# Performance work log

Hardware: AMD Instinct MI355X
Metric: run time of the kernel (lower is better)

The kernel has to match this reference:

```python
import jax, jax.numpy as jnp
import numpy as np

NUM_CLASSES = 1000
DIM = 256
N = 400000
MOMENTUM = 0.9


def setup_inputs() -> dict:
    key = jax.random.key(0)
    k1, k2, k3 = jax.random.split(key, 3)
    grads = jax.random.normal(k1, (N, DIM), dtype=jnp.float32)
    labels = jax.random.randint(k2, (N,), 0, NUM_CLASSES)
    # centroids buffer in its steady (initialized=True) state
    centroids = jax.random.normal(k3, (NUM_CLASSES, DIM), dtype=jnp.float32) * 0.1
    return {"grads": grads, "labels": labels, "centroids": centroids}


def reference(grads, labels, centroids):
    # --- update_centroids: per-class masked mean + EMA, as one segment-reduce ---
    sums = jax.ops.segment_sum(grads, labels, num_segments=NUM_CLASSES)            # [C, D]
    counts = jax.ops.segment_sum(jnp.ones((grads.shape[0],), grads.dtype), labels,
                                 num_segments=NUM_CLASSES)                          # [C]
    class_means = sums / jnp.maximum(counts, 1.0)[:, None]                          # [C, D]
    present = (counts > 0)[:, None]
    new_centroids = jnp.where(present,
                              MOMENTUM * centroids + (1.0 - MOMENTUM) * class_means,
                              centroids)                                            # classes with no samples keep old centroid

    # --- purify: rank-1 projection removing the first principal direction ---
    centered = new_centroids - new_centroids.mean(axis=0, keepdims=True)            # [C, D]
    _, _, Vh = jnp.linalg.svd(centered, full_matrices=False)
    v_y = Vh[0]                                                                     # [D]
    proj = (grads @ v_y)[:, None] * v_y[None, :]                                    # [N, D]
    return grads - proj
```

## Files before the change

### kernel.cpp

```cpp
#include <hip/hip_runtime.h>

#define N_ROWS 400000
#define DIM 256
#define NCLS 1000
#define NSQ 8

#define NB_S 256
#define NT_S 512
#define NBE  64
#define NTE  1024
#define NB_P 2048
#define NT_P 256
#define TOTW_P (NB_P * (NT_P / 64))

typedef float f4 __attribute__((ext_vector_type(4)));

#define OFF_BAR     0
#define OFF_BAR2    64
#define OFF_COUNTS  1024
#define OFF_COLSUM  5120
#define OFF_MAXBUF  6144
#define ZERO_BYTES  6208
#define OFF_BASE    6208
#define OFF_CURSOR  10304
#define OFF_V       14400
#define OFF_IDX     15424
#define OFF_NC      1615424
#define OFF_NCT     2639424
#define OFF_MA      3663424
#define OFF_MB      3925568

template <int NBLK>
__device__ __forceinline__ void grid_bar(unsigned* bar, int& phase) {
  __syncthreads();
  if (threadIdx.x == 0) {
    ++phase;
    __threadfence();
    __hip_atomic_fetch_add(bar, 1u, __ATOMIC_RELAXED, __HIP_MEMORY_SCOPE_AGENT);
    const unsigned target = (unsigned)NBLK * (unsigned)phase;
    while (__hip_atomic_load(bar, __ATOMIC_RELAXED, __HIP_MEMORY_SCOPE_AGENT) < target)
      __builtin_amdgcn_s_sleep(8);
    __threadfence();
  }
  __syncthreads();
}

__global__ __launch_bounds__(NT_S) void k_sort(const int* __restrict__ labels,
                                               char* __restrict__ ws) {
  unsigned* bar    = (unsigned*)(ws + OFF_BAR);
  unsigned* counts = (unsigned*)(ws + OFF_COUNTS);
  unsigned* base   = (unsigned*)(ws + OFF_BASE);
  unsigned* cursor = (unsigned*)(ws + OFF_CURSOR);
  unsigned* idx    = (unsigned*)(ws + OFF_IDX);

  __shared__ unsigned su[1024];
  const int t = threadIdx.x, b = blockIdx.x;
  int phase = 0;

  for (int i = t; i < NCLS; i += NT_S) su[i] = 0u;
  __syncthreads();
  for (int i = b*NT_S + t; i < N_ROWS; i += NB_S*NT_S)
    atomicAdd(&su[labels[i]], 1u);
  __syncthreads();
  for (int i = t; i < NCLS; i += NT_S) { unsigned v = su[i]; if (v) atomicAdd(&counts[i], v); }
  grid_bar<NB_S>(bar, phase);

  if (b == 0) {
    su[t] = counts[t]; su[t+512] = counts[t+512];
    int offset = 1;
    for (int d = 512; d > 0; d >>= 1) {
      __syncthreads();
      if (t < d) { int ai = offset*(2*t+1)-1, bi = offset*(2*t+2)-1; su[bi] += su[ai]; }
      offset <<= 1;
    }
    __syncthreads();
    if (t == 0) su[1023] = 0u;
    for (int d = 1; d < 1024; d <<= 1) {
      offset >>= 1;
      __syncthreads();
      if (t < d) { int ai = offset*(2*t+1)-1, bi = offset*(2*t+2)-1;
                   unsigned tm = su[ai]; su[ai] = su[bi]; su[bi] += tm; }
    }
    __syncthreads();
    base[t] = su[t]; cursor[t] = su[t];
    base[t+512] = su[t+512]; cursor[t+512] = su[t+512];
  }
  grid_bar<NB_S>(bar, phase);

  for (int i = b*NT_S + t; i < N_ROWS; i += NB_S*NT_S) {
    unsigned p = atomicAdd(&cursor[labels[i]], 1u);
    idx[p] = (unsigned)i;
  }
}

__global__ __launch_bounds__(512) void k_reduce(const float* __restrict__ grads,
                                                const unsigned* __restrict__ idx,
                                                const unsigned* __restrict__ base,
                                                const unsigned* __restrict__ counts,
                                                const float* __restrict__ centroids,
                                                float* __restrict__ NC,
                                                float* __restrict__ NCT,
                                                float* __restrict__ colsum) {
  const int cls = blockIdx.x;
  const unsigned s0 = base[cls], n = counts[cls];
  const int wave = threadIdx.x >> 6, lane = threadIdx.x & 63;
  const float4* g4 = (const float4*)grads;
  float4 acc = make_float4(0.f, 0.f, 0.f, 0.f);
  unsigned u = (unsigned)wave;
  for (; u + 24 < n; u += 32) {
    unsigned r0 = idx[s0+u],    r1 = idx[s0+u+8];
    unsigned r2 = idx[s0+u+16], r3 = idx[s0+u+24];
    float4 a = g4[(size_t)r0*64 + lane];
    float4 c = g4[(size_t)r1*64 + lane];
    float4 d = g4[(size_t)r2*64 + lane];
    float4 e = g4[(size_t)r3*64 + lane];
    acc.x += (a.x + c.x) + (d.x + e.x);
    acc.y += (a.y + c.y) + (d.y + e.y);
    acc.z += (a.z + c.z) + (d.z + e.z);
    acc.w += (a.w + c.w) + (d.w + e.w);
  }
  for (; u < n; u += 8) {
    unsigned r0 = idx[s0+u];
    float4 a = g4[(size_t)r0*64 + lane];
    acc.x += a.x; acc.y += a.y; acc.z += a.z; acc.w += a.w;
  }
  __shared__ float4 tmp[8][64];
  tmp[wave][lane] = acc;
  __syncthreads();
  const int d = threadIdx.x;
  if (d < DIM) {
    const float* tf = (const float*)tmp;
    float s = 0.f;
    #pragma unroll
    for (int w2 = 0; w2 < 8; ++w2) s += tf[w2*256 + d];
    float mean = s / fmaxf((float)n, 1.0f);
    float ce = centroids[cls*DIM + d];
    float ncv = (n > 0u) ? (0.9f*ce + 0.1f*mean) : ce;
    NC[cls*DIM + d]  = ncv;
    NCT[d*NCLS + cls] = ncv;
    atomicAdd(&colsum[d], ncv);
  }
}

__global__ __launch_bounds__(NTE) void k_eigen(char* __restrict__ ws) {
  unsigned* bar2   = (unsigned*)(ws + OFF_BAR2);
  float*    colsum = (float*)(ws + OFF_COLSUM);
  unsigned* maxbuf = (unsigned*)(ws + OFF_MAXBUF);
  float*    vfin   = (float*)(ws + OFF_V);
  float*    NC     = (float*)(ws + OFF_NC);
  float*    NCT    = (float*)(ws + OFF_NCT);
  float*    MA     = (float*)(ws + OFF_MA);
  float*    MB     = (float*)(ws + OFF_MB);

  __shared__ float scol[4][NCLS];
  __shared__ float sf[4][NTE];
  __shared__ float sx[DIM], sy[DIM];
  __shared__ int   sidx[256];
  __shared__ unsigned smax;

  const int t = threadIdx.x, b = blockIdx.x;
  const int i = t & 255, h = t >> 8;
  int phase = 0;

  {
    #pragma unroll
    for (int q = 0; q < 4; ++q)
      if (t < NCLS) scol[q][t] = NCT[(size_t)(b + 64*q)*NCLS + t];
    if (t == 0) smax = 0u;
    __syncthreads();
    float a0 = 0.f, a1 = 0.f, a2 = 0.f, a3 = 0.f;
    const int k0 = h * 250;
    #pragma unroll 5
    for (int k = k0; k < k0 + 250; ++k) {
      float nv = NC[k*DIM + i];
      a0 += nv * scol[0][k]; a1 += nv * scol[1][k];
      a2 += nv * scol[2][k]; a3 += nv * scol[3][k];
    }
    sf[0][t] = a0; sf[1][t] = a1; sf[2][t] = a2; sf[3][t] = a3;
    __syncthreads();
    if (h == 0) {
      float am = 0.f;
      #pragma unroll
      for (int q = 0; q < 4; ++q) {
        const int j = b + 64*q;
        float v = sf[q][i]+sf[q][i+256]+sf[q][i+512]+sf[q][i+768]
                - colsum[i]*colsum[j]*(1.0f/NCLS);
        MA[j*DIM + i] = v;
        am = fmaxf(am, fabsf(v));
      }
      #pragma unroll
      for (int m = 1; m < 64; m <<= 1) am = fmaxf(am, __shfl_xor(am, m, 64));
      if ((t & 63) == 0) atomicMax(&smax, __float_as_uint(am));
    }
    __syncthreads();
    if (t == 0) atomicMax(maxbuf, smax);
  }
  grid_bar<NBE>(bar2, phase);

  for (int st = 0; st < NSQ; ++st) {
    const float* A = (st & 1) ? MB : MA;
    float*       C = (st & 1) ? MA : MB;
    const float inv = 1.0f / __uint_as_float(maxbuf[st]);
    #pragma unroll
    for (int q = 0; q < 4; ++q)
      if (t < DIM) scol[q][t] = A[(b + 64*q)*DIM + t];
    if (t == 0) smax = 0u;
    __syncthreads();
    float a0 = 0.f, a1 = 0.f, a2 = 0.f, a3 = 0.f;
    const int k0 = h * 64;
    #pragma unroll 8
    for (int k = k0; k < k0 + 64; ++k) {
      float av = A[k*DIM + i];
      a0 += av * scol[0][k]; a1 += av * scol[1][k];
      a2 += av * scol[2][k]; a3 += av * scol[3][k];
    }
    sf[0][t] = a0; sf[1][t] = a1; sf[2][t] = a2; sf[3][t] = a3;
    __syncthreads();
    if (h == 0) {
      float am = 0.f;
      #pragma unroll
      for (int q = 0; q < 4; ++q) {
        const int j = b + 64*q;
        float v = (sf[q][i]+sf[q][i+256]+sf[q][i+512]+sf[q][i+768]) * inv * inv;
        C[j*DIM + i] = v;
        am = fmaxf(am, fabsf(v));
      }
      #pragma unroll
      for (int m = 1; m < 64; m <<= 1) am = fmaxf(am, __shfl_xor(am, m, 64));
      if ((t & 63) == 0) atomicMax(&smax, __float_as_uint(am));
    }
    __syncthreads();
    if (t == 0) atomicMax(&maxbuf[st+1], smax);
    grid_bar<NBE>(bar2, phase);
  }

  if (b == 0) {
    const int k0 = h * 64;
    float ns = 0.f;
    for (int k = k0; k < k0 + 64; ++k) { float x = MA[k*DIM + i]; ns += x*x; }
    sf[0][t] = ns;
    __syncthreads();
    if (h == 0) {
      scol[0][i] = sf[0][i]+sf[0][i+256]+sf[0][i+512]+sf[0][i+768];
      sidx[i] = i;
    }
    __syncthreads();
    for (int s = 128; s > 0; s >>= 1) {
      if (t < s && scol[0][t+s] > scol[0][t]) { scol[0][t] = scol[0][t+s]; sidx[t] = sidx[t+s]; }
      __syncthreads();
    }
    const int jm = sidx[0];
    const float nrm = sqrtf(fmaxf(scol[0][0], 1e-30f));
    __syncthreads();
    if (t < DIM) sx[t] = MA[(size_t)jm*DIM + t] / nrm;
    __syncthreads();
    for (int it = 0; it < 3; ++it) {
      float a2 = 0.f;
      #pragma unroll 8
      for (int k = k0; k < k0 + 64; ++k) a2 += MA[k*DIM + i] * sx[k];
      sf[0][t] = a2;
      __syncthreads();
      if (h == 0) {
        float yv = sf[0][i]+sf[0][i+256]+sf[0][i+512]+sf[0][i+768];
        sy[i] = yv;
        float q = yv*yv;
        #pragma unroll
        for (int m = 1; m < 64; m <<= 1) q += __shfl_xor(q, m, 64);
        if ((i & 63) == 0) scol[0][i >> 6] = q;
      }
      __syncthreads();
      const float innrm = rsqrtf(fmaxf(scol[0][0]+scol[0][1]+scol[0][2]+scol[0][3], 1e-30f));
      if (t < DIM) sx[t] = sy[t] * innrm;
      __syncthreads();
    }
    if (t < DIM) vfin[t] = sx[t];
  }
}

__global__ __launch_bounds__(NT_P) void k_project(const f4* __restrict__ g4,
                                                  const float* __restrict__ v,
                                                  f4* __restrict__ out) {
  const int lane = threadIdx.x & 63;
  const f4 v4 = ((const f4*)v)[lane];
  const int w = blockIdx.x * (NT_P/64) + (threadIdx.x >> 6);
  int r = w;
  for (; r + TOTW_P < N_ROWS; r += 2*TOTW_P) {
    f4 a = __builtin_nontemporal_load(&g4[(size_t)r*64 + lane]);
    f4 c = __builtin_nontemporal_load(&g4[(size_t)(r+TOTW_P)*64 + lane]);
    float da = a.x*v4.x + a.y*v4.y + a.z*v4.z + a.w*v4.w;
    float db = c.x*v4.x + c.y*v4.y + c.z*v4.z + c.w*v4.w;
    #pragma unroll
    for (int m = 1; m < 64; m <<= 1) { da += __shfl_xor(da, m, 64); db += __shfl_xor(db, m, 64); }
    f4 o0 = a - da * v4;
    f4 o1 = c - db * v4;
    __builtin_nontemporal_store(o0, &out[(size_t)r*64 + lane]);
    __builtin_nontemporal_store(o1, &out[(size_t)(r+TOTW_P)*64 + lane]);
  }
  for (; r < N_ROWS; r += TOTW_P) {
    f4 a = __builtin_nontemporal_load(&g4[(size_t)r*64 + lane]);
    float da = a.x*v4.x + a.y*v4.y + a.z*v4.z + a.w*v4.w;
    #pragma unroll
    for (int m = 1; m < 64; m <<= 1) da += __shfl_xor(da, m, 64);
    f4 o = a - da * v4;
    __builtin_nontemporal_store(o, &out[(size_t)r*64 + lane]);
  }
}

extern "C" void kernel_launch(void* const* d_in, const int* in_sizes, int n_in,
                              void* d_out, int out_size, void* d_ws, size_t ws_size,
                              hipStream_t stream) {
  const float* grads     = (const float*)d_in[0];
  const int*   labels    = (const int*)d_in[1];
  const float* centroids = (const float*)d_in[2];
  float* out = (float*)d_out;
  char* ws = (char*)d_ws;

  unsigned* idx    = (unsigned*)(ws + OFF_IDX);
  unsigned* counts = (unsigned*)(ws + OFF_COUNTS);
  unsigned* base   = (unsigned*)(ws + OFF_BASE);
  float*    colsum = (float*)(ws + OFF_COLSUM);
  float*    vfin   = (float*)(ws + OFF_V);
  float*    NC     = (float*)(ws + OFF_NC);
  float*    NCT    = (float*)(ws + OFF_NCT);

  (void)hipMemsetAsync(ws, 0, ZERO_BYTES, stream);

  k_sort<<<NB_S, NT_S, 0, stream>>>(labels, ws);
  k_reduce<<<NCLS, 512, 0, stream>>>(grads, idx, base, counts, centroids, NC, NCT, colsum);
  k_eigen<<<NBE, NTE, 0, stream>>>(ws);
  k_project<<<NB_P, NT_P, 0, stream>>>((const f4*)grads, vfin, (f4*)out);
}
```

Baseline: 440.1 us.

## Cut squaring steps, add power-iteration polish, vectorize eigen kernel, drop colsum atomics

The repeated-squaring eigen solver goes from eight squarings to six, and the closing power iteration goes from three to eight steps, so fewer grid-wide barriers are needed. The eigen kernel's Gram and squaring matmuls now use float4 rows spread over 16 waves. Column sums are computed inside the eigen kernel rather than through 256k global atomics in the reduce kernel. The gather loads in the reduce kernel are marked nontemporal. With fewer squarings the spectral gap is amplified less, so the result leans more on the polish iterations to converge.

```diff
diff --git a/kernel.cpp b/kernel.cpp
--- a/kernel.cpp
+++ b/kernel.cpp
@@ -3,7 +3,8 @@
 #define N_ROWS 400000
 #define DIM 256
 #define NCLS 1000
-#define NSQ 8
+#define NSQ 6
+#define NPOLISH 8
 
 #define NB_S 256
 #define NT_S 512
@@ -18,7 +19,6 @@
 #define OFF_BAR     0
 #define OFF_BAR2    64
 #define OFF_COUNTS  1024
-#define OFF_COLSUM  5120
 #define OFF_MAXBUF  6144
 #define ZERO_BYTES  6208
 #define OFF_BASE    6208
@@ -99,32 +99,27 @@
                                                 const unsigned* __restrict__ counts,
                                                 const float* __restrict__ centroids,
                                                 float* __restrict__ NC,
-                                                float* __restrict__ NCT,
-                                                float* __restrict__ colsum) {
+                                                float* __restrict__ NCT) {
   const int cls = blockIdx.x;
   const unsigned s0 = base[cls], n = counts[cls];
   const int wave = threadIdx.x >> 6, lane = threadIdx.x & 63;
-  const float4* g4 = (const float4*)grads;
-  float4 acc = make_float4(0.f, 0.f, 0.f, 0.f);
+  const f4* g4 = (const f4*)grads;
+  f4 acc = {0.f, 0.f, 0.f, 0.f};
   unsigned u = (unsigned)wave;
   for (; u + 24 < n; u += 32) {
     unsigned r0 = idx[s0+u],    r1 = idx[s0+u+8];
     unsigned r2 = idx[s0+u+16], r3 = idx[s0+u+24];
-    float4 a = g4[(size_t)r0*64 + lane];
-    float4 c = g4[(size_t)r1*64 + lane];
-    float4 d = g4[(size_t)r2*64 + lane];
-    float4 e = g4[(size_t)r3*64 + lane];
-    acc.x += (a.x + c.x) + (d.x + e.x);
-    acc.y += (a.y + c.y) + (d.y + e.y);
-    acc.z += (a.z + c.z) + (d.z + e.z);
-    acc.w += (a.w + c.w) + (d.w + e.w);
+    f4 a = __builtin_nontemporal_load(&g4[(size_t)r0*64 + lane]);
+    f4 c = __builtin_nontemporal_load(&g4[(size_t)r1*64 + lane]);
+    f4 d = __builtin_nontemporal_load(&g4[(size_t)r2*64 + lane]);
+    f4 e = __builtin_nontemporal_load(&g4[(size_t)r3*64 + lane]);
+    acc += (a + c) + (d + e);
   }
   for (; u < n; u += 8) {
     unsigned r0 = idx[s0+u];
-    float4 a = g4[(size_t)r0*64 + lane];
-    acc.x += a.x; acc.y += a.y; acc.z += a.z; acc.w += a.w;
-  }
-  __shared__ float4 tmp[8][64];
+    acc += __builtin_nontemporal_load(&g4[(size_t)r0*64 + lane]);
+  }
+  __shared__ f4 tmp[8][64];
   tmp[wave][lane] = acc;
   __syncthreads();
   const int d = threadIdx.x;
@@ -138,13 +133,11 @@
     float ncv = (n > 0u) ? (0.9f*ce + 0.1f*mean) : ce;
     NC[cls*DIM + d]  = ncv;
     NCT[d*NCLS + cls] = ncv;
-    atomicAdd(&colsum[d], ncv);
   }
 }
 
 __global__ __launch_bounds__(NTE) void k_eigen(char* __restrict__ ws) {
   unsigned* bar2   = (unsigned*)(ws + OFF_BAR2);
-  float*    colsum = (float*)(ws + OFF_COLSUM);
   unsigned* maxbuf = (unsigned*)(ws + OFF_MAXBUF);
   float*    vfin   = (float*)(ws + OFF_V);
   float*    NC     = (float*)(ws + OFF_NC);
@@ -152,128 +145,171 @@
   float*    MA     = (float*)(ws + OFF_MA);
   float*    MB     = (float*)(ws + OFF_MB);
 
-  __shared__ float scol[4][NCLS];
-  __shared__ float sf[4][NTE];
-  __shared__ float sx[DIM], sy[DIM];
+  __shared__ float scol[4][1024];
+  __shared__ f4    sacc[4][16][64];
+  __shared__ f4    scs[16][64];
+  __shared__ float colsumv[256];
+  __shared__ float red[256];
   __shared__ int   sidx[256];
+  __shared__ float sx[256], sy[256];
   __shared__ unsigned smax;
 
   const int t = threadIdx.x, b = blockIdx.x;
-  const int i = t & 255, h = t >> 8;
+  const int wave = t >> 6, lane = t & 63;
   int phase = 0;
-
+  const f4* NC4 = (const f4*)NC;
+
+  #pragma unroll
+  for (int q = 0; q < 4; ++q)
+    for (int k = t; k < NCLS; k += NTE) scol[q][k] = NCT[(size_t)(b + 64*q)*NCLS + k];
+  if (t == 0) smax = 0u;
+  __syncthreads();
   {
-    #pragma unroll
-    for (int q = 0; q < 4; ++q)
-      if (t < NCLS) scol[q][t] = NCT[(size_t)(b + 64*q)*NCLS + t];
-    if (t == 0) smax = 0u;
-    __syncthreads();
-    float a0 = 0.f, a1 = 0.f, a2 = 0.f, a3 = 0.f;
-    const int k0 = h * 250;
-    #pragma unroll 5
-    for (int k = k0; k < k0 + 250; ++k) {
-      float nv = NC[k*DIM + i];
+    f4 a0 = {0,0,0,0}, a1 = {0,0,0,0}, a2 = {0,0,0,0}, a3 = {0,0,0,0}, cs = {0,0,0,0};
+    for (int k = wave; k < NCLS; k += 16) {
+      f4 nv = NC4[(size_t)k*64 + lane];
       a0 += nv * scol[0][k]; a1 += nv * scol[1][k];
       a2 += nv * scol[2][k]; a3 += nv * scol[3][k];
-    }
-    sf[0][t] = a0; sf[1][t] = a1; sf[2][t] = a2; sf[3][t] = a3;
-    __syncthreads();
-    if (h == 0) {
-      float am = 0.f;
+      cs += nv;
+    }
+    sacc[0][wave][lane] = a0; sacc[1][wave][lane] = a1;
+    sacc[2][wave][lane] = a2; sacc[3][wave][lane] = a3;
+    scs[wave][lane] = cs;
+  }
+  __syncthreads();
+  float c0 = 0, c1 = 0, c2 = 0, c3 = 0;
+  if (t < 256) {
+    const float* p0 = (const float*)sacc[0]; const float* p1 = (const float*)sacc[1];
+    const float* p2 = (const float*)sacc[2]; const float* p3 = (const float*)sacc[3];
+    const float* pc = (const float*)scs;
+    float cc = 0;
+    #pragma unroll
+    for (int w2 = 0; w2 < 16; ++w2) {
+      c0 += p0[w2*256 + t]; c1 += p1[w2*256 + t];
+      c2 += p2[w2*256 + t]; c3 += p3[w2*256 + t];
+      cc += pc[w2*256 + t];
+    }
+    colsumv[t] = cc;
+  }
+  __syncthreads();
+  if (t < 256) {
+    const float inC = 1.0f / NCLS;
+    const float cst = colsumv[t];
+    float v0 = c0 - cst*colsumv[b      ]*inC;
+    float v1 = c1 - cst*colsumv[b +  64]*inC;
+    float v2 = c2 - cst*colsumv[b + 128]*inC;
+    float v3 = c3 - cst*colsumv[b + 192]*inC;
+    MA[(size_t)(b      )*DIM + t] = v0;
+    MA[(size_t)(b +  64)*DIM + t] = v1;
+    MA[(size_t)(b + 128)*DIM + t] = v2;
+    MA[(size_t)(b + 192)*DIM + t] = v3;
+    float am = fmaxf(fmaxf(fabsf(v0), fabsf(v1)), fmaxf(fabsf(v2), fabsf(v3)));
+    #pragma unroll
+    for (int m = 1; m < 64; m <<= 1) am = fmaxf(am, __shfl_xor(am, m, 64));
+    if ((t & 63) == 0) atomicMax(&smax, __float_as_uint(am));
+  }
+  __syncthreads();
+  if (t == 0) atomicMax(maxbuf, smax);
+  grid_bar<NBE>(bar2, phase);
+
+  for (int st = 0; st < NSQ; ++st) {
+    const float* A = (st & 1) ? MB : MA;
+    float*       C = (st & 1) ? MA : MB;
+    const f4* A4 = (const f4*)A;
+    const float inv = 1.0f / __uint_as_float(maxbuf[st]);
+    if (t < 256) {
+      scol[0][t] = A[(size_t)(b      )*DIM + t];
+      scol[1][t] = A[(size_t)(b +  64)*DIM + t];
+      scol[2][t] = A[(size_t)(b + 128)*DIM + t];
+      scol[3][t] = A[(size_t)(b + 192)*DIM + t];
+    }
+    if (t == 0) smax = 0u;
+    __syncthreads();
+    {
+      f4 a0 = {0,0,0,0}, a1 = {0,0,0,0}, a2 = {0,0,0,0}, a3 = {0,0,0,0};
+      for (int k = wave; k < DIM; k += 16) {
+        f4 av = A4[(size_t)k*64 + lane];
+        a0 += av * scol[0][k]; a1 += av * scol[1][k];
+        a2 += av * scol[2][k]; a3 += av * scol[3][k];
+      }
+      sacc[0][wave][lane] = a0; sacc[1][wave][lane] = a1;
+      sacc[2][wave][lane] = a2; sacc[3][wave][lane] = a3;
+    }
+    __syncthreads();
+    float d0 = 0, d1 = 0, d2 = 0, d3 = 0;
+    if (t < 256) {
+      const float* p0 = (const float*)sacc[0]; const float* p1 = (const float*)sacc[1];
+      const float* p2 = (const float*)sacc[2]; const float* p3 = (const float*)sacc[3];
       #pragma unroll
-      for (int q = 0; q < 4; ++q) {
-        const int j = b + 64*q;
-        float v = sf[q][i]+sf[q][i+256]+sf[q][i+512]+sf[q][i+768]
-                - colsum[i]*colsum[j]*(1.0f/NCLS);
-        MA[j*DIM + i] = v;
-        am = fmaxf(am, fabsf(v));
+      for (int w2 = 0; w2 < 16; ++w2) {
+        d0 += p0[w2*256 + t]; d1 += p1[w2*256 + t];
+        d2 += p2[w2*256 + t]; d3 += p3[w2*256 + t];
       }
+      const float i2 = inv * inv;
+      float v0 = d0*i2, v1 = d1*i2, v2 = d2*i2, v3 = d3*i2;
+      C[(size_t)(b      )*DIM + t] = v0;
+      C[(size_t)(b +  64)*DIM + t] = v1;
+      C[(size_t)(b + 128)*DIM + t] = v2;
+      C[(size_t)(b + 192)*DIM + t] = v3;
+      float am = fmaxf(fmaxf(fabsf(v0), fabsf(v1)), fmaxf(fabsf(v2), fabsf(v3)));
       #pragma unroll
       for (int m = 1; m < 64; m <<= 1) am = fmaxf(am, __shfl_xor(am, m, 64));
       if ((t & 63) == 0) atomicMax(&smax, __float_as_uint(am));
     }
     __syncthreads();
-    if (t == 0) atomicMax(maxbuf, smax);
-  }
-  grid_bar<NBE>(bar2, phase);
-
-  for (int st = 0; st < NSQ; ++st) {
-    const float* A = (st & 1) ? MB : MA;
-    float*       C = (st & 1) ? MA : MB;
-    const float inv = 1.0f / __uint_as_float(maxbuf[st]);
-    #pragma unroll
-    for (int q = 0; q < 4; ++q)
-      if (t < DIM) scol[q][t] = A[(b + 64*q)*DIM + t];
-    if (t == 0) smax = 0u;
-    __syncthreads();
-    float a0 = 0.f, a1 = 0.f, a2 = 0.f, a3 = 0.f;
-    const int k0 = h * 64;
-    #pragma unroll 8
-    for (int k = k0; k < k0 + 64; ++k) {
-      float av = A[k*DIM + i];
-      a0 += av * scol[0][k]; a1 += av * scol[1][k];
-      a2 += av * scol[2][k]; a3 += av * scol[3][k];
-    }
-    sf[0][t] = a0; sf[1][t] = a1; sf[2][t] = a2; sf[3][t] = a3;
-    __syncthreads();
-    if (h == 0) {
-      float am = 0.f;
-      #pragma unroll
-      for (int q = 0; q < 4; ++q) {
-        const int j = b + 64*q;
-        float v = (sf[q][i]+sf[q][i+256]+sf[q][i+512]+sf[q][i+768]) * inv * inv;
-        C[j*DIM + i] = v;
-        am = fmaxf(am, fabsf(v));
-      }
-      #pragma unroll
-      for (int m = 1; m < 64; m <<= 1) am = fmaxf(am, __shfl_xor(am, m, 64));
-      if ((t & 63) == 0) atomicMax(&smax, __float_as_uint(am));
-    }
-    __syncthreads();
     if (t == 0) atomicMax(&maxbuf[st+1], smax);
     grid_bar<NBE>(bar2, phase);
   }
 
   if (b == 0) {
-    const int k0 = h * 64;
-    float ns = 0.f;
-    for (int k = k0; k < k0 + 64; ++k) { float x = MA[k*DIM + i]; ns += x*x; }
-    sf[0][t] = ns;
-    __syncthreads();
-    if (h == 0) {
-      scol[0][i] = sf[0][i]+sf[0][i+256]+sf[0][i+512]+sf[0][i+768];
-      sidx[i] = i;
-    }
-    __syncthreads();
-    for (int s = 128; s > 0; s >>= 1) {
-      if (t < s && scol[0][t+s] > scol[0][t]) { scol[0][t] = scol[0][t+s]; sidx[t] = sidx[t+s]; }
+    const float* M = MA;
+    const f4* M4 = (const f4*)MA;
+    {
+      f4 na = {0,0,0,0};
+      for (int k = wave; k < DIM; k += 16) { f4 av = M4[(size_t)k*64 + lane]; na += av*av; }
+      sacc[0][wave][lane] = na;
+    }
+    __syncthreads();
+    if (t < 256) {
+      const float* p0 = (const float*)sacc[0];
+      float s = 0;
+      #pragma unroll
+      for (int w2 = 0; w2 < 16; ++w2) s += p0[w2*256 + t];
+      red[t] = s; sidx[t] = t;
+    }
+    __syncthreads();
+    for (int s2 = 128; s2 > 0; s2 >>= 1) {
+      if (t < s2 && red[t+s2] > red[t]) { red[t] = red[t+s2]; sidx[t] = sidx[t+s2]; }
       __syncthreads();
     }
     const int jm = sidx[0];
-    const float nrm = sqrtf(fmaxf(scol[0][0], 1e-30f));
-    __syncthreads();
-    if (t < DIM) sx[t] = MA[(size_t)jm*DIM + t] / nrm;
-    __syncthreads();
-    for (int it = 0; it < 3; ++it) {
-      float a2 = 0.f;
-      #pragma unroll 8
-      for (int k = k0; k < k0 + 64; ++k) a2 += MA[k*DIM + i] * sx[k];
-      sf[0][t] = a2;
-      __syncthreads();
-      if (h == 0) {
-        float yv = sf[0][i]+sf[0][i+256]+sf[0][i+512]+sf[0][i+768];
-        sy[i] = yv;
-        float q = yv*yv;
+    const float nrm = sqrtf(fmaxf(red[0], 1e-30f));
+    __syncthreads();
+    if (t < 256) sx[t] = M[(size_t)jm*DIM + t] / nrm;
+    __syncthreads();
+    for (int it = 0; it < NPOLISH; ++it) {
+      f4 ya = {0,0,0,0};
+      for (int k = wave; k < DIM; k += 16) { f4 av = M4[(size_t)k*64 + lane]; ya += av * sx[k]; }
+      sacc[0][wave][lane] = ya;
+      __syncthreads();
+      if (t < 256) {
+        const float* p0 = (const float*)sacc[0];
+        float s = 0;
         #pragma unroll
-        for (int m = 1; m < 64; m <<= 1) q += __shfl_xor(q, m, 64);
-        if ((i & 63) == 0) scol[0][i >> 6] = q;
+        for (int w2 = 0; w2 < 16; ++w2) s += p0[w2*256 + t];
+        sy[t] = s; red[t] = s*s;
       }
       __syncthreads();
-      const float innrm = rsqrtf(fmaxf(scol[0][0]+scol[0][1]+scol[0][2]+scol[0][3], 1e-30f));
-      if (t < DIM) sx[t] = sy[t] * innrm;
-      __syncthreads();
-    }
-    if (t < DIM) vfin[t] = sx[t];
+      for (int s2 = 128; s2 > 0; s2 >>= 1) {
+        if (t < s2) red[t] += red[t+s2];
+        __syncthreads();
+      }
+      const float innrm = rsqrtf(fmaxf(red[0], 1e-30f));
+      __syncthreads();
+      if (t < 256) sx[t] = sy[t] * innrm;
+      __syncthreads();
+    }
+    if (t < 256) vfin[t] = sx[t];
   }
 }
 
@@ -318,7 +354,6 @@
   unsigned* idx    = (unsigned*)(ws + OFF_IDX);
   unsigned* counts = (unsigned*)(ws + OFF_COUNTS);
   unsigned* base   = (unsigned*)(ws + OFF_BASE);
-  float*    colsum = (float*)(ws + OFF_COLSUM);
   float*    vfin   = (float*)(ws + OFF_V);
   float*    NC     = (float*)(ws + OFF_NC);
   float*    NCT    = (float*)(ws + OFF_NCT);
@@ -326,7 +361,7 @@
   (void)hipMemsetAsync(ws, 0, ZERO_BYTES, stream);
 
   k_sort<<<NB_S, NT_S, 0, stream>>>(labels, ws);
-  k_reduce<<<NCLS, 512, 0, stream>>>(grads, idx, base, counts, centroids, NC, NCT, colsum);
+  k_reduce<<<NCLS, 512, 0, stream>>>(grads, idx, base, counts, centroids, NC, NCT);
   k_eigen<<<NBE, NTE, 0, stream>>>(ws);
   k_project<<<NB_P, NT_P, 0, stream>>>((const f4*)grads, vfin, (f4*)out);
 }
```

After: 468.5 us. 6.4% more time.
